# Kernel optimization log

Hardware: AMD Instinct MI355X
Metric: run time of the kernel (lower is better)

Reference implementation:

```python
import jax, jax.numpy as jnp
from jax import lax
import numpy as np
import math

EPS = 1e-5
LEVELS = 17  # quantized levels round(x*255/16) for x in [0,1) -> 0..16


def _bn(x, g, b):
    # training-mode BatchNorm2d: batch statistics over (B,H,W), biased var
    m = x.mean(axis=(0, 2, 3), keepdims=True)
    v = x.var(axis=(0, 2, 3), keepdims=True)
    return (x - m) / jnp.sqrt(v + EPS) * g[None, :, None, None] + b[None, :, None, None]


def _mode_pool_11(x):
    # x is pre-quantized to k*16/256, k in 0..16 -> sliding-window mode via per-level counts
    q = jnp.round(x * 16.0).astype(jnp.int32)  # recover integer level k
    qp = jnp.pad(q, ((0, 0), (0, 0), (5, 5), (5, 5)), mode='reflect')
    oh = (qp[:, :, None, :, :] == jnp.arange(LEVELS, dtype=jnp.int32)[None, None, :, None, None]).astype(jnp.float32)  # [B,C,L,H+10,W+10]
    counts = lax.reduce_window(oh, 0.0, lax.add, (1, 1, 1, 11, 11), (1, 1, 1, 1, 1), 'VALID')  # [B,C,L,H,W]
    lvl = jnp.argmax(counts, axis=2)  # ties -> smallest level, matching torch.mode
    return lvl.astype(x.dtype) * (16.0 / 256.0)


def setup_inputs() -> dict:
    key = jax.random.key(0)
    ks = jax.random.split(key, 8)
    B, C, H, W, F = 2, 3, 512, 512, 16
    x = jax.random.uniform(ks[0], (B, C, H, W), jnp.float32)
    w1 = jax.random.normal(ks[1], (F, C), jnp.float32) * 0.1
    b1 = jnp.zeros((F,), jnp.float32)
    g1 = jnp.ones((F,), jnp.float32); be1 = jnp.zeros((F,), jnp.float32)
    w2 = jax.random.normal(ks[2], (F, F), jnp.float32) * 0.1
    b2 = jnp.zeros((F,), jnp.float32)
    g2 = jnp.ones((F,), jnp.float32); be2 = jnp.zeros((F,), jnp.float32)
    dw = jax.random.normal(ks[3], (F, 1, 3, 3), jnp.float32) * 0.1  # depthwise 3x3
    gd = jnp.ones((F,), jnp.float32); bd = jnp.zeros((F,), jnp.float32)
    ww = jax.random.normal(ks[4], (F,), jnp.float32) * 0.1  # depthwise 1x1 = per-channel scale
    gw = jnp.ones((F,), jnp.float32); bw = jnp.zeros((F,), jnp.float32)
    wh = jax.random.normal(ks[5], (F,), jnp.float32) * 0.1
    gh = jnp.ones((F,), jnp.float32); bh = jnp.zeros((F,), jnp.float32)
    return dict(x=x, w1=w1, b1=b1, g1=g1, be1=be1, w2=w2, b2=b2, g2=g2, be2=be2,
                dw=dw, gd=gd, bd=bd, ww=ww, gw=gw, bw=bw, wh=wh, gh=gh, bh=bh)


def reference(x, w1, b1, g1, be1, w2, b2, g2, be2, dw, gd, bd, ww, gw, bw, wh, gh, bh):
    lrelu = jax.nn.leaky_relu  # default slope 0.01 matches torch LeakyReLU
    x = jnp.round(x * 255.0 / 16.0) * 16.0 / 256.0  # quantize to 16-ish levels
    x = _mode_pool_11(x)
    B, C, H, W = x.shape
    F = w1.shape[0]
    # prepare: two 1x1 conv + BN + LeakyReLU blocks
    p = jnp.einsum('oc,bchw->bohw', w1, x) + b1[None, :, None, None]
    p = lrelu(_bn(p, g1, be1))
    p = jnp.einsum('oc,bchw->bohw', w2, p) + b2[None, :, None, None]
    p = lrelu(_bn(p, g2, be2))
    inter = jnp.stack([p, p], axis=0).reshape(B, 2 * F, H, W)  # mirrors torch stack(dim=0).reshape
    d = p
    n = math.floor(math.log(min(H, W), 3))
    for _ in range(n):
        d = lax.conv_general_dilated(d, dw, (1, 1), 'SAME', feature_group_count=F,
                                     dimension_numbers=('NCHW', 'OIHW', 'NCHW'))
        d = lrelu(_bn(d, gd, bd))
        wdt = lrelu(_bn(d * ww[None, :, None, None], gw, bw))
        hgt = lrelu(_bn(d * wh[None, :, None, None], gh, bh))
        sc = jnp.stack([wdt, hgt], axis=1).reshape(B, 2 * F, H, W)
        inter = sc + inter
    return inter
```

## Files before the change

### kernel.cpp

```cpp
#include <hip/hip_runtime.h>
#include <hip/hip_bf16.h>
#include <stdint.h>
#include <stddef.h>

#define HW 262144
#define EPSF 1e-5f

typedef __hip_bfloat16 bf16;

__device__ __forceinline__ float us2f(uint32_t u){
  union { uint32_t i; float f; } c; c.i = u << 16; return c.f;
}
__device__ __forceinline__ ushort f2bu(float v){
  union { bf16 h; ushort u; } c; c.h = __float2bfloat16(v); return c.u;
}
__device__ __forceinline__ float lrelu(float v){ return v > 0.0f ? v : 0.01f * v; }
__device__ __forceinline__ uint32_t umax2(uint32_t a, uint32_t b){ return a > b ? a : b; }

__global__ __launch_bounds__(256) void k_quant_pad(const float* __restrict__ x,
                                                   uint8_t* __restrict__ qpad){
  int idx = blockIdx.x * 256 + threadIdx.x;
  if (idx >= 6 * 522 * 522) return;
  int pw = idx % 522; int t = idx / 522; int ph = t % 522; int img = t / 522;
  int h = ph - 5; h = h < 0 ? -h : h; if (h > 511) h = 1022 - h;
  int w = pw - 5; w = w < 0 ? -w : w; if (w > 511) w = 1022 - w;
  float v = x[img * HW + h * 512 + w];
  int k = (int)rintf((v * 255.0f) / 16.0f);
  qpad[img * (522 * 528) + ph * 528 + pw] = (uint8_t)k;
}

__global__ __launch_bounds__(256) void k_mode(const uint8_t* __restrict__ qpad,
                                              uint8_t* __restrict__ xm){
  __shared__ uint8_t tile[14 * 528];
  int tid = threadIdx.x;
  int img = blockIdx.x >> 7;
  int h0  = (blockIdx.x & 127) << 2;
  {
    const uint4* g4 = (const uint4*)(qpad + img * (522 * 528) + h0 * 528);
    uint4* t4 = (uint4*)tile;
    t4[tid] = g4[tid];
    if (tid < 206) t4[tid + 256] = g4[tid + 256];
  }
  __syncthreads();
  int r4 = tid >> 6;
  int w0 = (tid & 63) << 3;
  const uint8_t* base = tile + r4 * 528 + w0;
  uint32_t c0 = 0, c1 = 0, c2 = 0, c3 = 0, c4 = 0;
#define HINC(q) { uint32_t inc_ = 1u << (((q) & 3u) << 3); uint32_t rr_ = (q) >> 2; \
    c0 += (rr_==0u)?inc_:0u; c1 += (rr_==1u)?inc_:0u; c2 += (rr_==2u)?inc_:0u; \
    c3 += (rr_==3u)?inc_:0u; c4 += (rr_==4u)?inc_:0u; }
#define HDEC(q) { uint32_t inc_ = 1u << (((q) & 3u) << 3); uint32_t rr_ = (q) >> 2; \
    c0 -= (rr_==0u)?inc_:0u; c1 -= (rr_==1u)?inc_:0u; c2 -= (rr_==2u)?inc_:0u; \
    c3 -= (rr_==3u)?inc_:0u; c4 -= (rr_==4u)?inc_:0u; }
  #pragma unroll 1
  for (int r = 0; r < 11; ++r){
    const uint8_t* row = base + r * 528;
    #pragma unroll
    for (int j = 0; j < 11; ++j){ uint32_t q = row[j]; HINC(q); }
  }
  uint64_t packed = 0;
  #pragma unroll 1
  for (int s = 0; s < 8; ++s){
#define KEY(reg, sh, l) (((((reg) >> (sh)) & 0xffu) << 5) | (16u - (uint32_t)(l)))
    uint32_t m0 = umax2(umax2(KEY(c0,0,0),  KEY(c0,8,1)),  umax2(KEY(c0,16,2),  KEY(c0,24,3)));
    uint32_t m1 = umax2(umax2(KEY(c1,0,4),  KEY(c1,8,5)),  umax2(KEY(c1,16,6),  KEY(c1,24,7)));
    uint32_t m2 = umax2(umax2(KEY(c2,0,8),  KEY(c2,8,9)),  umax2(KEY(c2,16,10), KEY(c2,24,11)));
    uint32_t m3 = umax2(umax2(KEY(c3,0,12), KEY(c3,8,13)), umax2(KEY(c3,16,14), KEY(c3,24,15)));
    uint32_t m  = umax2(umax2(umax2(m0, m1), umax2(m2, m3)), KEY(c4,0,16));
#undef KEY
    uint32_t lvl = 16u - (m & 31u);
    packed |= ((uint64_t)lvl) << (8 * s);
    if (s < 7){
      #pragma unroll
      for (int r = 0; r < 11; ++r){
        uint32_t qo = base[r * 528 + s];      HDEC(qo);
        uint32_t qn = base[r * 528 + s + 11]; HINC(qn);
      }
    }
  }
#undef HINC
#undef HDEC
  *(uint64_t*)(xm + img * HW + (h0 + r4) * 512 + w0) = packed;
}

__device__ __forceinline__ void reduce16(float* su, float* sq, float* __restrict__ partials){
  __shared__ float lsum[32];
  int tid = threadIdx.x;
  if (tid < 32) lsum[tid] = 0.0f;
  __syncthreads();
  #pragma unroll
  for (int o = 0; o < 16; ++o){
    float s = su[o], q = sq[o];
    #pragma unroll
    for (int off = 32; off >= 1; off >>= 1){
      s += __shfl_xor(s, off);
      q += __shfl_xor(q, off);
    }
    if ((tid & 63) == 0){ atomicAdd(&lsum[o], s); atomicAdd(&lsum[16 + o], q); }
  }
  __syncthreads();
  if (tid < 32) partials[blockIdx.x * 32 + tid] = lsum[tid];
}

__global__ __launch_bounds__(256) void k_stats1(const uint8_t* __restrict__ xm,
                                                const float* __restrict__ w1,
                                                const float* __restrict__ b1,
                                                float* __restrict__ partials){
  int t0 = (blockIdx.x * 256 + threadIdx.x) << 2;
  int b = t0 >> 18, hw = t0 & (HW - 1);
  uint32_t q0 = *(const uint32_t*)(xm + (b * 3 + 0) * HW + hw);
  uint32_t q1 = *(const uint32_t*)(xm + (b * 3 + 1) * HW + hw);
  uint32_t q2 = *(const uint32_t*)(xm + (b * 3 + 2) * HW + hw);
  float su[16], sq[16];
  #pragma unroll
  for (int o = 0; o < 16; ++o){ su[o] = 0.0f; sq[o] = 0.0f; }
  #pragma unroll
  for (int px = 0; px < 4; ++px){
    float x0 = (float)((q0 >> (8 * px)) & 0xffu) * 0.0625f;
    float x1 = (float)((q1 >> (8 * px)) & 0xffu) * 0.0625f;
    float x2 = (float)((q2 >> (8 * px)) & 0xffu) * 0.0625f;
    #pragma unroll
    for (int o = 0; o < 16; ++o){
      float v = b1[o] + w1[o*3]*x0 + w1[o*3+1]*x1 + w1[o*3+2]*x2;
      su[o] += v; sq[o] += v * v;
    }
  }
  reduce16(su, sq, partials);
}

__global__ __launch_bounds__(256) void k_stats2(const uint8_t* __restrict__ xm,
                                                const float* __restrict__ w1,
                                                const float* __restrict__ b1,
                                                const float* __restrict__ w2,
                                                const float* __restrict__ b2,
                                                const float* __restrict__ params,
                                                float* __restrict__ partials){
  int t0 = (blockIdx.x * 256 + threadIdx.x) << 2;
  int b = t0 >> 18, hw = t0 & (HW - 1);
  uint32_t q0 = *(const uint32_t*)(xm + (b * 3 + 0) * HW + hw);
  uint32_t q1 = *(const uint32_t*)(xm + (b * 3 + 1) * HW + hw);
  uint32_t q2 = *(const uint32_t*)(xm + (b * 3 + 2) * HW + hw);
  float tv[4][16];
  #pragma unroll
  for (int px = 0; px < 4; ++px){
    float x0 = (float)((q0 >> (8 * px)) & 0xffu) * 0.0625f;
    float x1 = (float)((q1 >> (8 * px)) & 0xffu) * 0.0625f;
    float x2 = (float)((q2 >> (8 * px)) & 0xffu) * 0.0625f;
    #pragma unroll
    for (int o = 0; o < 16; ++o){
      float v = b1[o] + w1[o*3]*x0 + w1[o*3+1]*x1 + w1[o*3+2]*x2;
      tv[px][o] = lrelu(v * params[o] + params[16 + o]);
    }
  }
  float su[16], sq[16];
  #pragma unroll
  for (int o = 0; o < 16; ++o){ su[o] = 0.0f; sq[o] = 0.0f; }
  #pragma unroll
  for (int o = 0; o < 16; ++o){
    #pragma unroll
    for (int px = 0; px < 4; ++px){
      float acc = b2[o];
      #pragma unroll
      for (int c = 0; c < 16; ++c) acc = fmaf(w2[o*16 + c], tv[px][c], acc);
      su[o] += acc; sq[o] += acc * acc;
    }
  }
  reduce16(su, sq, partials);
}

__global__ __launch_bounds__(256) void k_prep(const uint8_t* __restrict__ xm,
                                              const float* __restrict__ w1,
                                              const float* __restrict__ b1,
                                              const float* __restrict__ w2,
                                              const float* __restrict__ b2,
                                              const float* __restrict__ params,
                                              bf16* __restrict__ p){
  int t0 = (blockIdx.x * 256 + threadIdx.x) << 2;
  int b = t0 >> 18, hw = t0 & (HW - 1);
  uint32_t q0 = *(const uint32_t*)(xm + (b * 3 + 0) * HW + hw);
  uint32_t q1 = *(const uint32_t*)(xm + (b * 3 + 1) * HW + hw);
  uint32_t q2 = *(const uint32_t*)(xm + (b * 3 + 2) * HW + hw);
  float tv[4][16];
  #pragma unroll
  for (int px = 0; px < 4; ++px){
    float x0 = (float)((q0 >> (8 * px)) & 0xffu) * 0.0625f;
    float x1 = (float)((q1 >> (8 * px)) & 0xffu) * 0.0625f;
    float x2 = (float)((q2 >> (8 * px)) & 0xffu) * 0.0625f;
    #pragma unroll
    for (int o = 0; o < 16; ++o){
      float v = b1[o] + w1[o*3]*x0 + w1[o*3+1]*x1 + w1[o*3+2]*x2;
      tv[px][o] = lrelu(v * params[o] + params[16 + o]);
    }
  }
  #pragma unroll
  for (int o = 0; o < 16; ++o){
    uint32_t w01 = 0, w23 = 0;
    #pragma unroll
    for (int px = 0; px < 4; ++px){
      float acc = b2[o];
      #pragma unroll
      for (int c = 0; c < 16; ++c) acc = fmaf(w2[o*16 + c], tv[px][c], acc);
      float v = lrelu(acc * params[32 + o] + params[48 + o]);
      uint32_t bits = (uint32_t)f2bu(v);
      if (px == 0) w01 = bits;
      else if (px == 1) w01 |= bits << 16;
      else if (px == 2) w23 = bits;
      else w23 |= bits << 16;
    }
    uint2 ov; ov.x = w01; ov.y = w23;
    *(uint2*)((ushort*)p + (b * 16 + o) * HW + hw) = ov;
  }
}

__device__ __forceinline__ void load_row10(const ushort* __restrict__ rp, int w0, float* v){
  uint4 cc = *(const uint4*)(rp + w0);
  uint32_t l = (w0 == 0)   ? 0u : (uint32_t)rp[w0 - 1];
  uint32_t r = (w0 == 504) ? 0u : (uint32_t)rp[w0 + 8];
  v[0] = us2f(l);
  v[1] = us2f(cc.x & 0xffffu); v[2] = us2f(cc.x >> 16);
  v[3] = us2f(cc.y & 0xffffu); v[4] = us2f(cc.y >> 16);
  v[5] = us2f(cc.z & 0xffffu); v[6] = us2f(cc.z >> 16);
  v[7] = us2f(cc.w & 0xffffu); v[8] = us2f(cc.w >> 16);
  v[9] = us2f(r);
}

__device__ __forceinline__ void zero_row10(float* v){
  #pragma unroll
  for (int j = 0; j < 10; ++j) v[j] = 0.0f;
}

__device__ __forceinline__ void reduce2(float s, float q, float* __restrict__ partials){
  __shared__ float l2[2];
  int tid = threadIdx.x;
  if (tid < 2) l2[tid] = 0.0f;
  __syncthreads();
  #pragma unroll
  for (int off = 32; off >= 1; off >>= 1){
    s += __shfl_xor(s, off);
    q += __shfl_xor(q, off);
  }
  if ((tid & 63) == 0){ atomicAdd(&l2[0], s); atomicAdd(&l2[1], q); }
  __syncthreads();
  if (tid < 2) partials[blockIdx.x * 2 + tid] = l2[tid];
}

__global__ __launch_bounds__(256) void k_convstat(const bf16* __restrict__ d,
                                                  const float* __restrict__ dw,
                                                  float* __restrict__ P1,
                                                  bf16* __restrict__ cout){
  int bid = blockIdx.x;
  int plane = bid >> 7, rg = bid & 127;
  int f = plane & 15;
  int tid = threadIdx.x;
  int h  = (rg << 2) + (tid >> 6);
  int w0 = (tid & 63) << 3;
  const ushort* pl = (const ushort*)d + plane * HW;
  float wf[9];
  #pragma unroll
  for (int i = 0; i < 9; ++i) wf[i] = dw[f * 9 + i];
  float v[3][10];
  #pragma unroll
  for (int dy = 0; dy < 3; ++dy){
    int row = h + dy - 1;
    if ((unsigned)row < 512u) load_row10(pl + row * 512, w0, v[dy]);
    else zero_row10(v[dy]);
  }
  float s = 0.0f, q = 0.0f;
  uint32_t cb[4];
  #pragma unroll
  for (int k = 0; k < 8; ++k){
    float acc = 0.0f;
    #pragma unroll
    for (int dy = 0; dy < 3; ++dy)
      #pragma unroll
      for (int dx = 0; dx < 3; ++dx)
        acc = fmaf(wf[dy*3 + dx], v[dy][k + dx], acc);
    s += acc; q += acc * acc;
    uint32_t bits = (uint32_t)f2bu(acc);
    if ((k & 1) == 0) cb[k >> 1] = bits; else cb[k >> 1] |= bits << 16;
  }
  uint4 cv; cv.x = cb[0]; cv.y = cb[1]; cv.z = cb[2]; cv.w = cb[3];
  *(uint4*)((ushort*)cout + plane * HW + h * 512 + w0) = cv;
  reduce2(s, q, P1);
}

__device__ __forceinline__ void chan_sum_wave(const float* __restrict__ P, int f, int lane,
                                              double& S, double& Q){
  S = 0.0; Q = 0.0;
  #pragma unroll
  for (int i = 0; i < 4; ++i){
    int e = lane + i * 64;
    int blk = (((e >> 7) * 16 + f) << 7) + (e & 127);
    S += (double)P[blk * 2];
    Q += (double)P[blk * 2 + 1];
  }
  #pragma unroll
  for (int off = 32; off >= 1; off >>= 1){
    S += __shfl_xor(S, off);
    Q += __shfl_xor(Q, off);
  }
}

__global__ __launch_bounds__(256) void k_bnfused(const bf16* __restrict__ cin,
                                                 const float* __restrict__ dw,
                                                 const float* __restrict__ gd,
                                                 const float* __restrict__ bd,
                                                 const float* __restrict__ P1in,
                                                 bf16* __restrict__ cout,
                                                 float* __restrict__ P2out,
                                                 float* __restrict__ P1out,
                                                 float* __restrict__ dparams,
                                                 int t, int write_c){
  __shared__ ushort strip[6][512];
  __shared__ float acc4[4];
  int bid = blockIdx.x;
  int plane = bid >> 7, rg = bid & 127;
  int f = plane & 15;
  int tid = threadIdx.x;

  double S, Q;
  chan_sum_wave(P1in, f, tid & 63, S, Q);
  float sc, sh;
  {
    double m = S / 524288.0;
    double v = Q / 524288.0 - m * m;
    sc = gd[f] / sqrtf((float)v + EPSF);
    sh = bd[f] - (float)m * sc;
  }
  if (plane < 16 && rg == 0 && tid == 0){
    dparams[512 + t * 32 + 2 * f]     = sc;
    dparams[512 + t * 32 + 2 * f + 1] = sh;
  }
  if (tid < 4) acc4[tid] = 0.0f;

  int h0 = rg << 2;
  int h  = h0 + (tid >> 6);
  int w0 = (tid & 63) << 3;
  const ushort* cpl = (const ushort*)cin + plane * HW;

  float s2 = 0.0f, q2 = 0.0f;
  {
    uint4 cv = *(const uint4*)(cpl + h * 512 + w0);
    float cf[8];
    cf[0] = us2f(cv.x & 0xffffu); cf[1] = us2f(cv.x >> 16);
    cf[2] = us2f(cv.y & 0xffffu); cf[3] = us2f(cv.y >> 16);
    cf[4] = us2f(cv.z & 0xffffu); cf[5] = us2f(cv.z >> 16);
    cf[6] = us2f(cv.w & 0xffffu); cf[7] = us2f(cv.w >> 16);
    uint32_t ob[4];
    #pragma unroll
    for (int k = 0; k < 8; ++k){
      float vv = lrelu(fmaf(cf[k], sc, sh));
      uint32_t bits = (uint32_t)f2bu(vv);
      if ((k & 1) == 0) ob[k >> 1] = bits; else ob[k >> 1] |= bits << 16;
      s2 += vv; q2 += vv * vv;
    }
    uint4 ov; ov.x = ob[0]; ov.y = ob[1]; ov.z = ob[2]; ov.w = ob[3];
    *(uint4*)&strip[1 + (tid >> 6)][w0] = ov;
  }

  if (tid < 128){
    int hh = (tid < 64) ? (h0 - 1) : (h0 + 4);
    int si = (tid < 64) ? 0 : 5;
    int wh0 = (tid & 63) << 3;
    uint4 hv; hv.x = 0; hv.y = 0; hv.z = 0; hv.w = 0;
    if ((unsigned)hh < 512u){
      uint4 cv = *(const uint4*)(cpl + hh * 512 + wh0);
      float cf[8];
      cf[0] = us2f(cv.x & 0xffffu); cf[1] = us2f(cv.x >> 16);
      cf[2] = us2f(cv.y & 0xffffu); cf[3] = us2f(cv.y >> 16);
      cf[4] = us2f(cv.z & 0xffffu); cf[5] = us2f(cv.z >> 16);
      cf[6] = us2f(cv.w & 0xffffu); cf[7] = us2f(cv.w >> 16);
      uint32_t hb[4];
      #pragma unroll
      for (int k = 0; k < 8; ++k){
        float vv = lrelu(fmaf(cf[k], sc, sh));
        uint32_t bits = (uint32_t)f2bu(vv);
        if ((k & 1) == 0) hb[k >> 1] = bits; else hb[k >> 1] |= bits << 16;
      }
      hv.x = hb[0]; hv.y = hb[1]; hv.z = hb[2]; hv.w = hb[3];
    }
    *(uint4*)&strip[si][wh0] = hv;
  }
  __syncthreads();

  float wf[9];
  #pragma unroll
  for (int i = 0; i < 9; ++i) wf[i] = dw[f * 9 + i];
  float s1 = 0.0f, q1 = 0.0f;
  {
    int si = 1 + (tid >> 6);
    float v[3][10];
    #pragma unroll
    for (int dy = 0; dy < 3; ++dy)
      load_row10(&strip[si - 1 + dy][0], w0, v[dy]);
    uint32_t cb[4];
    #pragma unroll
    for (int k = 0; k < 8; ++k){
      float acc = 0.0f;
      #pragma unroll
      for (int dy = 0; dy < 3; ++dy)
        #pragma unroll
        for (int dx = 0; dx < 3; ++dx)
          acc = fmaf(wf[dy*3 + dx], v[dy][k + dx], acc);
      s1 += acc; q1 += acc * acc;
      uint32_t bits = (uint32_t)f2bu(acc);
      if ((k & 1) == 0) cb[k >> 1] = bits; else cb[k >> 1] |= bits << 16;
    }
    if (write_c){
      uint4 cv2; cv2.x = cb[0]; cv2.y = cb[1]; cv2.z = cb[2]; cv2.w = cb[3];
      *(uint4*)((ushort*)cout + plane * HW + h * 512 + w0) = cv2;
    }
  }

  #pragma unroll
  for (int off = 32; off >= 1; off >>= 1){
    s2 += __shfl_xor(s2, off);
    q2 += __shfl_xor(q2, off);
    s1 += __shfl_xor(s1, off);
    q1 += __shfl_xor(q1, off);
  }
  if ((tid & 63) == 0){
    atomicAdd(&acc4[0], s2); atomicAdd(&acc4[1], q2);
    atomicAdd(&acc4[2], s1); atomicAdd(&acc4[3], q1);
  }
  __syncthreads();
  if (tid < 2)      P2out[bid * 2 + tid]       = acc4[tid];
  else if (tid < 4) P1out[bid * 2 + (tid - 2)] = acc4[tid];
}

__global__ __launch_bounds__(256) void k_fin_prep(const float* __restrict__ partials,
                                                  const float* __restrict__ g,
                                                  const float* __restrict__ bb,
                                                  float* __restrict__ params,
                                                  int offS, int offT){
  int tid = threadIdx.x;
  int o = tid & 15, c = tid >> 4;
  double S = 0.0, Q = 0.0;
  for (int i = c * 32; i < (c + 1) * 32; ++i){
    S += (double)partials[i * 32 + o];
    Q += (double)partials[i * 32 + 16 + o];
  }
  __shared__ double lS[256], lQ[256];
  lS[tid] = S; lQ[tid] = Q; __syncthreads();
  for (int st = 8; st >= 1; st >>= 1){
    if (c < st){ lS[tid] += lS[tid + st * 16]; lQ[tid] += lQ[tid + st * 16]; }
    __syncthreads();
  }
  if (tid < 16){
    double m = lS[tid] / 524288.0;
    double v = lQ[tid] / 524288.0 - m * m;
    float sc = g[tid] / sqrtf((float)v + EPSF);
    params[offS + tid] = sc;
    params[offT + tid] = bb[tid] - (float)m * sc;
  }
}

__global__ __launch_bounds__(256) void k_fin_all(const float* __restrict__ P2,
                                                 const float* __restrict__ ww,
                                                 const float* __restrict__ gw,
                                                 const float* __restrict__ bw,
                                                 const float* __restrict__ wh,
                                                 const float* __restrict__ gh,
                                                 const float* __restrict__ bh,
                                                 float* __restrict__ dparams){
  int tid = threadIdx.x;
  int wid = tid >> 6, lane = tid & 63;
  int pair = blockIdx.x * 4 + wid;
  int t = pair >> 4, f = pair & 15;
  double S, Q;
  chan_sum_wave(P2 + t * 8192, f, lane, S, Q);
  if (lane == 0){
    float m = (float)(S / 524288.0);
    float v = (float)(Q / 524288.0) - m * m;
    float sw = ww[f] * gw[f] / sqrtf(ww[f] * ww[f] * v + EPSF);
    float tw = bw[f] - m * sw;
    float s2 = wh[f] * gh[f] / sqrtf(wh[f] * wh[f] * v + EPSF);
    float t2 = bh[f] - m * s2;
    dparams[t * 64 + f]      = sw;
    dparams[t * 64 + 16 + f] = tw;
    dparams[t * 64 + 32 + f] = s2;
    dparams[t * 64 + 48 + f] = t2;
  }
}

__device__ __forceinline__ void conv8(uint4 cc, float* v){
  v[0] = us2f(cc.x & 0xffffu); v[1] = us2f(cc.x >> 16);
  v[2] = us2f(cc.y & 0xffffu); v[3] = us2f(cc.y >> 16);
  v[4] = us2f(cc.z & 0xffffu); v[5] = us2f(cc.z >> 16);
  v[6] = us2f(cc.w & 0xffffu); v[7] = us2f(cc.w >> 16);
}

__global__ __launch_bounds__(256) void k_final(const bf16* __restrict__ p,
                                               const bf16* __restrict__ c1,
                                               const bf16* __restrict__ c2,
                                               const bf16* __restrict__ c3,
                                               const bf16* __restrict__ c4,
                                               const bf16* __restrict__ c5,
                                               const float* __restrict__ dparams,
                                               float* __restrict__ out){
  int tid = threadIdx.x;
  int f = blockIdx.x >> 7;
  int gid = blockIdx.x * 256 + tid;
  int hw = (gid & 32767) << 3;
  int fo = f * HW + hw;
  int f1 = (16 + f) * HW + hw;

  uint4 rp0 = *(const uint4*)((const ushort*)p + fo);
  uint4 rp1 = *(const uint4*)((const ushort*)p + f1);
  uint4 r0a = *(const uint4*)((const ushort*)c1 + fo);
  uint4 r0b = *(const uint4*)((const ushort*)c1 + f1);
  uint4 r1a = *(const uint4*)((const ushort*)c2 + fo);
  uint4 r1b = *(const uint4*)((const ushort*)c2 + f1);
  uint4 r2a = *(const uint4*)((const ushort*)c3 + fo);
  uint4 r2b = *(const uint4*)((const ushort*)c3 + f1);
  uint4 r3a = *(const uint4*)((const ushort*)c4 + fo);
  uint4 r3b = *(const uint4*)((const ushort*)c4 + f1);
  uint4 r4a = *(const uint4*)((const ushort*)c5 + fo);
  uint4 r4b = *(const uint4*)((const ushort*)c5 + f1);

  float swA[5], twA[5], shA[5], thA[5], scA[5], sbA[5];
  #pragma unroll
  for (int t = 0; t < 5; ++t){
    swA[t] = dparams[t * 64 + f];
    twA[t] = dparams[t * 64 + 16 + f];
    shA[t] = dparams[t * 64 + 32 + f];
    thA[t] = dparams[t * 64 + 48 + f];
    scA[t] = dparams[512 + t * 32 + 2 * f];
    sbA[t] = dparams[512 + t * 32 + 2 * f + 1];
  }

  float pf[8], pg[8];
  conv8(rp0, pf); conv8(rp1, pg);
  float a00[8], a01[8], a10[8], a11[8];
  #pragma unroll
  for (int k = 0; k < 8; ++k){ a00[k] = pf[k]; a01[k] = pg[k]; a10[k] = pf[k]; a11[k] = pg[k]; }

  uint4 ra[5] = { r0a, r1a, r2a, r3a, r4a };
  uint4 rb[5] = { r0b, r1b, r2b, r3b, r4b };
  #pragma unroll
  for (int t = 0; t < 5; ++t){
    float cv0[8], cv1[8];
    conv8(ra[t], cv0); conv8(rb[t], cv1);
    float sw = swA[t], tw = twA[t], sh = shA[t], th = thA[t];
    float sc = scA[t], sb = sbA[t];
    #pragma unroll
    for (int k = 0; k < 8; ++k){
      float dv0 = lrelu(fmaf(cv0[k], sc, sb));
      float dv1 = lrelu(fmaf(cv1[k], sc, sb));
      a00[k] += lrelu(fmaf(dv0, sw, tw));
      a01[k] += lrelu(fmaf(dv0, sh, th));
      a10[k] += lrelu(fmaf(dv1, sw, tw));
      a11[k] += lrelu(fmaf(dv1, sh, th));
    }
  }
  #pragma unroll
  for (int half = 0; half < 2; ++half){
    float4 v0 = { a00[half*4+0], a00[half*4+1], a00[half*4+2], a00[half*4+3] };
    float4 v1 = { a01[half*4+0], a01[half*4+1], a01[half*4+2], a01[half*4+3] };
    float4 v2 = { a10[half*4+0], a10[half*4+1], a10[half*4+2], a10[half*4+3] };
    float4 v3 = { a11[half*4+0], a11[half*4+1], a11[half*4+2], a11[half*4+3] };
    *(float4*)(out + f * HW + hw + half*4)        = v0;
    *(float4*)(out + (16 + f) * HW + hw + half*4) = v1;
    *(float4*)(out + (32 + f) * HW + hw + half*4) = v2;
    *(float4*)(out + (48 + f) * HW + hw + half*4) = v3;
  }
}

extern "C" void kernel_launch(void* const* d_in, const int* in_sizes, int n_in,
                              void* d_out, int out_size, void* d_ws, size_t ws_size,
                              hipStream_t stream){
  (void)in_sizes; (void)n_in; (void)out_size;
  const float* x   = (const float*)d_in[0];
  const float* w1  = (const float*)d_in[1];
  const float* b1  = (const float*)d_in[2];
  const float* g1  = (const float*)d_in[3];
  const float* be1 = (const float*)d_in[4];
  const float* w2  = (const float*)d_in[5];
  const float* b2  = (const float*)d_in[6];
  const float* g2  = (const float*)d_in[7];
  const float* be2 = (const float*)d_in[8];
  const float* dw  = (const float*)d_in[9];
  const float* gd  = (const float*)d_in[10];
  const float* bd  = (const float*)d_in[11];
  const float* ww  = (const float*)d_in[12];
  const float* gw  = (const float*)d_in[13];
  const float* bw  = (const float*)d_in[14];
  const float* wh  = (const float*)d_in[15];
  const float* gh  = (const float*)d_in[16];
  const float* bh  = (const float*)d_in[17];
  float* out = (float*)d_out;

  char* ws = (char*)d_ws;
  size_t off = 0;
  auto alloc = [&](size_t sz) -> void* {
    void* ptr = ws + off;
    off = (off + sz + 4095) & ~(size_t)4095;
    return ptr;
  };
  uint8_t* qpad  = (uint8_t*)alloc((size_t)6 * 522 * 528);
  uint8_t* xm    = (uint8_t*)alloc((size_t)6 * HW);
  bf16*    p     = (bf16*)   alloc((size_t)32 * HW * 2);
  bf16*    cbuf[5];
  for (int i = 0; i < 5; ++i) cbuf[i] = (bf16*)alloc((size_t)32 * HW * 2);
  float*   Pp     = (float*)  alloc((size_t)512 * 32 * 4);
  float*   P1a    = (float*)  alloc((size_t)4096 * 2 * 4);
  float*   P1b    = (float*)  alloc((size_t)4096 * 2 * 4);
  float*   P2     = (float*)  alloc((size_t)5 * 4096 * 2 * 4);
  float*   params = (float*)  alloc(4096);
  float*   dparams= (float*)  alloc(4096);
  if (ws_size < off) return;

  k_quant_pad<<<dim3((6*522*522 + 255)/256), dim3(256), 0, stream>>>(x, qpad);
  k_mode     <<<dim3(768), dim3(256), 0, stream>>>(qpad, xm);
  k_stats1   <<<dim3(512), dim3(256), 0, stream>>>(xm, w1, b1, Pp);
  k_fin_prep <<<dim3(1),   dim3(256), 0, stream>>>(Pp, g1, be1, params, 0, 16);
  k_stats2   <<<dim3(512), dim3(256), 0, stream>>>(xm, w1, b1, w2, b2, params, Pp);
  k_fin_prep <<<dim3(1),   dim3(256), 0, stream>>>(Pp, g2, be2, params, 32, 48);
  k_prep     <<<dim3(512), dim3(256), 0, stream>>>(xm, w1, b1, w2, b2, params, p);
  k_convstat <<<dim3(4096), dim3(256), 0, stream>>>(p, dw, P1a, cbuf[0]);

  float* Pin = P1a; float* Pout = P1b;
  for (int t = 0; t < 5; ++t){
    k_bnfused<<<dim3(4096), dim3(256), 0, stream>>>(
        cbuf[t], dw, gd, bd, Pin,
        (t < 4) ? cbuf[t + 1] : cbuf[0],
        P2 + t * 8192, Pout, dparams, t, (t < 4) ? 1 : 0);
    float* tmp = Pin; Pin = Pout; Pout = tmp;
  }
  k_fin_all<<<dim3(20), dim3(256), 0, stream>>>(P2, ww, gw, bw, wh, gh, bh, dparams);
  k_final<<<dim3(2048), dim3(256), 0, stream>>>(p, cbuf[0], cbuf[1], cbuf[2],
                                                cbuf[3], cbuf[4], dparams, out);
}
```

Before: 223.5 us.

## Fuse quantize-pad into mode kernel and fold BN finalize into consumers

The separate quantize-and-reflect-pad kernel is removed. The mode kernel now reads the float input directly, quantizes it and writes the padded tile into shared memory, which drops the qpad buffer round trip and one launch. The two single-block BN finalize kernels are also removed. Each block of stats2 and prep now reduces the 512 partials itself, which saves launches and serialized tiny kernels but repeats that reduction in every block and makes float loads in the mode kernel less vectorized.

```diff
diff --git a/kernel.cpp b/kernel.cpp
--- a/kernel.cpp
+++ b/kernel.cpp
@@ -17,29 +17,25 @@
 __device__ __forceinline__ float lrelu(float v){ return v > 0.0f ? v : 0.01f * v; }
 __device__ __forceinline__ uint32_t umax2(uint32_t a, uint32_t b){ return a > b ? a : b; }
 
-__global__ __launch_bounds__(256) void k_quant_pad(const float* __restrict__ x,
-                                                   uint8_t* __restrict__ qpad){
-  int idx = blockIdx.x * 256 + threadIdx.x;
-  if (idx >= 6 * 522 * 522) return;
-  int pw = idx % 522; int t = idx / 522; int ph = t % 522; int img = t / 522;
-  int h = ph - 5; h = h < 0 ? -h : h; if (h > 511) h = 1022 - h;
-  int w = pw - 5; w = w < 0 ? -w : w; if (w > 511) w = 1022 - w;
-  float v = x[img * HW + h * 512 + w];
-  int k = (int)rintf((v * 255.0f) / 16.0f);
-  qpad[img * (522 * 528) + ph * 528 + pw] = (uint8_t)k;
-}
-
-__global__ __launch_bounds__(256) void k_mode(const uint8_t* __restrict__ qpad,
+__global__ __launch_bounds__(256) void k_mode(const float* __restrict__ x,
                                               uint8_t* __restrict__ xm){
   __shared__ uint8_t tile[14 * 528];
   int tid = threadIdx.x;
   int img = blockIdx.x >> 7;
   int h0  = (blockIdx.x & 127) << 2;
   {
-    const uint4* g4 = (const uint4*)(qpad + img * (522 * 528) + h0 * 528);
-    uint4* t4 = (uint4*)tile;
-    t4[tid] = g4[tid];
-    if (tid < 206) t4[tid + 256] = g4[tid + 256];
+    const float* xp = x + img * HW;
+    #pragma unroll 1
+    for (int r = 0; r < 14; ++r){
+      int hs = h0 + r - 5; hs = hs < 0 ? -hs : hs; if (hs > 511) hs = 1022 - hs;
+      const float* row = xp + hs * 512;
+      for (int c = tid; c < 522; c += 256){
+        int ws = c - 5; ws = ws < 0 ? -ws : ws; if (ws > 511) ws = 1022 - ws;
+        float v = row[ws];
+        int k = (int)rintf((v * 255.0f) / 16.0f);
+        tile[r * 528 + c] = (uint8_t)k;
+      }
+    }
   }
   __syncthreads();
   int r4 = tid >> 6;
@@ -102,6 +98,39 @@
   if (tid < 32) partials[blockIdx.x * 32 + tid] = lsum[tid];
 }
 
+__device__ __forceinline__ void prep_params(const float* __restrict__ Pp,
+                                            const float* __restrict__ g,
+                                            const float* __restrict__ bb,
+                                            float* prm, float* partS, double* totS){
+  int tid = threadIdx.x;
+  int o = tid & 31, gg = tid >> 5;
+  float s0 = 0.0f, s1 = 0.0f, s2 = 0.0f, s3 = 0.0f;
+  #pragma unroll
+  for (int j = 0; j < 64; j += 4){
+    s0 += Pp[(gg * 64 + j    ) * 32 + o];
+    s1 += Pp[(gg * 64 + j + 1) * 32 + o];
+    s2 += Pp[(gg * 64 + j + 2) * 32 + o];
+    s3 += Pp[(gg * 64 + j + 3) * 32 + o];
+  }
+  partS[gg * 32 + o] = (s0 + s1) + (s2 + s3);
+  __syncthreads();
+  if (tid < 32){
+    double t = 0.0;
+    #pragma unroll
+    for (int k = 0; k < 8; ++k) t += (double)partS[k * 32 + tid];
+    totS[tid] = t;
+  }
+  __syncthreads();
+  if (tid < 16){
+    double m = totS[tid] / 524288.0;
+    double v = totS[16 + tid] / 524288.0 - m * m;
+    float sc = g[tid] / sqrtf((float)v + EPSF);
+    prm[tid] = sc;
+    prm[16 + tid] = bb[tid] - (float)m * sc;
+  }
+  __syncthreads();
+}
+
 __global__ __launch_bounds__(256) void k_stats1(const uint8_t* __restrict__ xm,
                                                 const float* __restrict__ w1,
                                                 const float* __restrict__ b1,
@@ -133,8 +162,14 @@
                                                 const float* __restrict__ b1,
                                                 const float* __restrict__ w2,
                                                 const float* __restrict__ b2,
-                                                const float* __restrict__ params,
-                                                float* __restrict__ partials){
+                                                const float* __restrict__ Pp1,
+                                                const float* __restrict__ g1,
+                                                const float* __restrict__ be1,
+                                                float* __restrict__ Pp2){
+  __shared__ float prm[32];
+  __shared__ float partS[8 * 32];
+  __shared__ double totS[32];
+  prep_params(Pp1, g1, be1, prm, partS, totS);
   int t0 = (blockIdx.x * 256 + threadIdx.x) << 2;
   int b = t0 >> 18, hw = t0 & (HW - 1);
   uint32_t q0 = *(const uint32_t*)(xm + (b * 3 + 0) * HW + hw);
@@ -149,7 +184,7 @@
     #pragma unroll
     for (int o = 0; o < 16; ++o){
       float v = b1[o] + w1[o*3]*x0 + w1[o*3+1]*x1 + w1[o*3+2]*x2;
-      tv[px][o] = lrelu(v * params[o] + params[16 + o]);
+      tv[px][o] = lrelu(v * prm[o] + prm[16 + o]);
     }
   }
   float su[16], sq[16];
@@ -165,7 +200,7 @@
       su[o] += acc; sq[o] += acc * acc;
     }
   }
-  reduce16(su, sq, partials);
+  reduce16(su, sq, Pp2);
 }
 
 __global__ __launch_bounds__(256) void k_prep(const uint8_t* __restrict__ xm,
@@ -173,8 +208,18 @@
                                               const float* __restrict__ b1,
                                               const float* __restrict__ w2,
                                               const float* __restrict__ b2,
-                                              const float* __restrict__ params,
+                                              const float* __restrict__ Pp1,
+                                              const float* __restrict__ g1,
+                                              const float* __restrict__ be1,
+                                              const float* __restrict__ Pp2,
+                                              const float* __restrict__ g2,
+                                              const float* __restrict__ be2,
                                               bf16* __restrict__ p){
+  __shared__ float prm1[32], prm2[32];
+  __shared__ float partS[8 * 32];
+  __shared__ double totS[32];
+  prep_params(Pp1, g1, be1, prm1, partS, totS);
+  prep_params(Pp2, g2, be2, prm2, partS, totS);
   int t0 = (blockIdx.x * 256 + threadIdx.x) << 2;
   int b = t0 >> 18, hw = t0 & (HW - 1);
   uint32_t q0 = *(const uint32_t*)(xm + (b * 3 + 0) * HW + hw);
@@ -189,7 +234,7 @@
     #pragma unroll
     for (int o = 0; o < 16; ++o){
       float v = b1[o] + w1[o*3]*x0 + w1[o*3+1]*x1 + w1[o*3+2]*x2;
-      tv[px][o] = lrelu(v * params[o] + params[16 + o]);
+      tv[px][o] = lrelu(v * prm1[o] + prm1[16 + o]);
     }
   }
   #pragma unroll
@@ -200,7 +245,7 @@
       float acc = b2[o];
       #pragma unroll
       for (int c = 0; c < 16; ++c) acc = fmaf(w2[o*16 + c], tv[px][c], acc);
-      float v = lrelu(acc * params[32 + o] + params[48 + o]);
+      float v = lrelu(acc * prm2[o] + prm2[16 + o]);
       uint32_t bits = (uint32_t)f2bu(v);
       if (px == 0) w01 = bits;
       else if (px == 1) w01 |= bits << 16;
@@ -426,33 +471,6 @@
   __syncthreads();
   if (tid < 2)      P2out[bid * 2 + tid]       = acc4[tid];
   else if (tid < 4) P1out[bid * 2 + (tid - 2)] = acc4[tid];
-}
-
-__global__ __launch_bounds__(256) void k_fin_prep(const float* __restrict__ partials,
-                                                  const float* __restrict__ g,
-                                                  const float* __restrict__ bb,
-                                                  float* __restrict__ params,
-                                                  int offS, int offT){
-  int tid = threadIdx.x;
-  int o = tid & 15, c = tid >> 4;
-  double S = 0.0, Q = 0.0;
-  for (int i = c * 32; i < (c + 1) * 32; ++i){
-    S += (double)partials[i * 32 + o];
-    Q += (double)partials[i * 32 + 16 + o];
-  }
-  __shared__ double lS[256], lQ[256];
-  lS[tid] = S; lQ[tid] = Q; __syncthreads();
-  for (int st = 8; st >= 1; st >>= 1){
-    if (c < st){ lS[tid] += lS[tid + st * 16]; lQ[tid] += lQ[tid + st * 16]; }
-    __syncthreads();
-  }
-  if (tid < 16){
-    double m = lS[tid] / 524288.0;
-    double v = lQ[tid] / 524288.0 - m * m;
-    float sc = g[tid] / sqrtf((float)v + EPSF);
-    params[offS + tid] = sc;
-    params[offT + tid] = bb[tid] - (float)m * sc;
-  }
 }
 
 __global__ __launch_bounds__(256) void k_fin_all(const float* __restrict__ P2,
@@ -597,26 +615,24 @@
     off = (off + sz + 4095) & ~(size_t)4095;
     return ptr;
   };
-  uint8_t* qpad  = (uint8_t*)alloc((size_t)6 * 522 * 528);
   uint8_t* xm    = (uint8_t*)alloc((size_t)6 * HW);
   bf16*    p     = (bf16*)   alloc((size_t)32 * HW * 2);
   bf16*    cbuf[5];
   for (int i = 0; i < 5; ++i) cbuf[i] = (bf16*)alloc((size_t)32 * HW * 2);
-  float*   Pp     = (float*)  alloc((size_t)512 * 32 * 4);
+  float*   Pp1    = (float*)  alloc((size_t)512 * 32 * 4);
+  float*   Pp2    = (float*)  alloc((size_t)512 * 32 * 4);
   float*   P1a    = (float*)  alloc((size_t)4096 * 2 * 4);
   float*   P1b    = (float*)  alloc((size_t)4096 * 2 * 4);
   float*   P2     = (float*)  alloc((size_t)5 * 4096 * 2 * 4);
-  float*   params = (float*)  alloc(4096);
   float*   dparams= (float*)  alloc(4096);
   if (ws_size < off) return;
 
-  k_quant_pad<<<dim3((6*522*522 + 255)/256), dim3(256), 0, stream>>>(x, qpad);
-  k_mode     <<<dim3(768), dim3(256), 0, stream>>>(qpad, xm);
-  k_stats1   <<<dim3(512), dim3(256), 0, stream>>>(xm, w1, b1, Pp);
-  k_fin_prep <<<dim3(1),   dim3(256), 0, stream>>>(Pp, g1, be1, params, 0, 16);
-  k_stats2   <<<dim3(512), dim3(256), 0, stream>>>(xm, w1, b1, w2, b2, params, Pp);
-  k_fin_prep <<<dim3(1),   dim3(256), 0, stream>>>(Pp, g2, be2, params, 32, 48);
-  k_prep     <<<dim3(512), dim3(256), 0, stream>>>(xm, w1, b1, w2, b2, params, p);
+  k_mode     <<<dim3(768), dim3(256), 0, stream>>>(x, xm);
+  k_stats1   <<<dim3(512), dim3(256), 0, stream>>>(xm, w1, b1, Pp1);
+  k_stats2   <<<dim3(512), dim3(256), 0, stream>>>(xm, w1, b1, w2, b2,
+                                                   Pp1, g1, be1, Pp2);
+  k_prep     <<<dim3(512), dim3(256), 0, stream>>>(xm, w1, b1, w2, b2,
+                                                   Pp1, g1, be1, Pp2, g2, be2, p);
   k_convstat <<<dim3(4096), dim3(256), 0, stream>>>(p, dw, P1a, cbuf[0]);
 
   float* Pin = P1a; float* Pout = P1b;
```

Result: faster. 210.3 us (-5.9%).
